# Performance work log

Hardware: AMD Instinct MI355X
Metric: run time of the kernel (lower is better)

Reference implementation:

```python
import jax, jax.numpy as jnp
import numpy as np

AGENT_RADIUS = 0.2
SAFETY_DIST = 0.1
_ang = np.linspace(0.0, 2.0 * np.pi, 8, endpoint=False)
OBSTACLES = np.stack([10.0 * np.cos(_ang), 10.0 * np.sin(_ang), 0.5 * np.ones(8)], axis=-1).astype(np.float32)  # (x, y, r)


def _qp_solve(p, G, h):
    """Exact solve of: min_z 0.5 z^T z + p^T z  s.t. G z <= h, z in R^2.
    Equivalent to QPFunction with Q=I. Enumerates KKT candidates over active
    sets of size 0, 1, 2 (closed form in 2D) and picks the feasible optimum.
    p: [2], G: [m,2], h: [m]."""
    m = G.shape[0]
    ii, jj = np.triu_indices(m, 1)
    # active set {} -> unconstrained minimizer
    z0 = -p[None, :]                                        # [1,2]
    # active set {i}: z = -p - lam*g_i, g_i.z = h_i
    gg = jnp.sum(G * G, axis=-1)                            # [m]
    lam1 = (-(G @ p) - h) / (gg + 1e-12)
    z1 = -p[None, :] - lam1[:, None] * G                    # [m,2]
    ok1 = lam1 >= -1e-8
    # active set {i,j}: z solves 2x2 system [g_i; g_j] z = [h_i; h_j]
    Gi, Gj = G[ii], G[jj]                                   # [P,2]
    hi, hj = h[ii], h[jj]
    det = Gi[:, 0] * Gj[:, 1] - Gi[:, 1] * Gj[:, 0]
    det_ok = jnp.abs(det) > 1e-9
    ds = jnp.where(det_ok, det, 1.0)
    zx = (hi * Gj[:, 1] - hj * Gi[:, 1]) / ds
    zy = (Gi[:, 0] * hj - Gj[:, 0] * hi) / ds
    z2 = jnp.stack([zx, zy], axis=-1)                       # [P,2]
    r = -(z2 + p[None, :])                                  # A^T lam = r
    lam_i = (Gj[:, 1] * r[:, 0] - Gj[:, 0] * r[:, 1]) / ds
    lam_j = (Gi[:, 0] * r[:, 1] - Gi[:, 1] * r[:, 0]) / ds
    ok2 = det_ok & (lam_i >= -1e-8) & (lam_j >= -1e-8)
    Z = jnp.concatenate([z0, z1, z2], axis=0)               # [K,2]
    ok = jnp.concatenate([jnp.ones((1,), bool), ok1, ok2], axis=0)
    tol = 1e-6 * (1.0 + jnp.abs(h))
    feas = jnp.all(Z @ G.T <= (h + tol)[None, :], axis=-1)  # [K]
    obj = 0.5 * jnp.sum(Z * Z, axis=-1) + Z @ p
    obj = jnp.where(ok & feas, obj, jnp.inf)
    return Z[jnp.argmin(obj)]


def _forward(x, mean, std, W1, b1, W21, b21, W31, b31, W22, b22, W32, b32):
    x0 = x * std + mean                                     # de-normalized state [B,8]
    hid = jax.nn.relu(x @ W1.T + b1)
    x31 = jax.nn.relu(hid @ W21.T + b21) @ W31.T + b31      # reference control p [B,2]
    x32 = 4.0 * jax.nn.sigmoid(jax.nn.relu(hid @ W22.T + b22) @ W32.T + b32)  # CBF penalties [B,2]
    px, py, theta, v = x0[:, 0], x0[:, 1], x0[:, 2], x0[:, 3]
    ox, oy, oth, ov = x0[:, 4], x0[:, 5], x0[:, 6], x0[:, 7]
    st, ct = jnp.sin(theta), jnp.cos(theta)
    vs, vc = v * st, v * ct
    obs = jnp.asarray(OBSTACLES, x.dtype)
    # static obstacle constraints, vectorized over the n_obs obstacles
    dx = px[:, None] - obs[None, :, 0]                      # [B,n_obs]
    dy = py[:, None] - obs[None, :, 1]
    R = AGENT_RADIUS + obs[:, 2] + SAFETY_DIST
    bar = dx * dx + dy * dy - (R * R)[None, :]
    bdot = 2.0 * dx * vc[:, None] + 2.0 * dy * vs[:, None]
    Lf2b = (2.0 * v * v)[:, None]
    u1 = -2.0 * dx * vs[:, None] + 2.0 * dy * vc[:, None]
    u2 = 2.0 * dx * ct[:, None] + 2.0 * dy * st[:, None]
    G_obs = -jnp.stack([u1, u2], axis=-1)                   # [B,n_obs,2]
    s0, s1 = x32[:, 0:1], x32[:, 1:2]
    h_obs = Lf2b + (s0 + s1) * bdot + (s0 * s1) * bar       # [B,n_obs]
    # opponent constraint
    Ro = 2.0 * AGENT_RADIUS + SAFETY_DIST
    dxo, dyo = px - ox, py - oy
    so, co = jnp.sin(oth), jnp.cos(oth)
    bar_o = dxo * dxo + dyo * dyo - Ro * Ro
    bdot_o = 2.0 * dxo * (vc - ov * co) + 2.0 * dyo * (vs - ov * so)
    Lf2b_o = 2.0 * (v * v + ov * ov + 2.0 * v * ov * jnp.cos(theta - oth))
    u1o = -2.0 * dxo * vs + 2.0 * dyo * vc
    u2o = 2.0 * dxo * ct + 2.0 * dyo * st
    G_opp = -jnp.stack([u1o, u2o], axis=-1)[:, None, :]     # [B,1,2]
    h_opp = (Lf2b_o + (x32[:, 0] + x32[:, 1]) * bdot_o + x32[:, 0] * x32[:, 1] * bar_o)[:, None]
    G = jnp.concatenate([G_obs, G_opp], axis=1)             # [B,m,2]
    h = jnp.concatenate([h_obs, h_opp], axis=1)             # [B,m]
    return jax.vmap(_qp_solve)(x31, G, h)                   # [B,2]


def setup_inputs() -> dict:
    key = jax.random.key(0)
    ks = jax.random.split(key, 6)
    B, nF, H1, H2 = 65536, 8, 256, 128

    def lin(k, o, i):
        k1, k2 = jax.random.split(k)
        W = jax.random.normal(k1, (o, i), jnp.float32) / np.float32(np.sqrt(i))
        b = jax.random.normal(k2, (o,), jnp.float32) * 0.01
        return W, b

    W1, b1 = lin(ks[0], H1, nF)
    W21, b21 = lin(ks[1], H2, H1)
    W31, b31 = lin(ks[2], 2, H2)
    W22, b22 = lin(ks[3], H2, H1)
    W32, b32 = lin(ks[4], 2, H2)
    x = jax.random.normal(ks[5], (B, nF), jnp.float32)
    return {"x": x, "mean": jnp.zeros((nF,), jnp.float32), "std": jnp.ones((nF,), jnp.float32),
            "W1": W1, "b1": b1, "W21": W21, "b21": b21, "W31": W31, "b31": b31,
            "W22": W22, "b22": b22, "W32": W32, "b32": b32, "sgn": 1}


def reference(x, mean, std, W1, b1, W21, b21, W31, b31, W22, b22, W32, b32, sgn):
    # sgn==1 / training path -> batched differentiable QP solve
    return _forward(x, mean, std, W1, b1, W21, b21, W31, b31, W22, b22, W32, b32)
```

## Files before the change

### kernel.cpp

```cpp
#include <hip/hip_runtime.h>
#include <math.h>


typedef unsigned int u32;
typedef unsigned short u16;
typedef __attribute__((ext_vector_type(8))) short short8;
typedef __attribute__((ext_vector_type(4))) float f32x4;
typedef __attribute__((ext_vector_type(2))) float f32x2;
typedef __attribute__((ext_vector_type(4))) u32 u32x4;

union Frag { short8 v; u32 u[4]; u32x4 q; };

__device__ __forceinline__ u16 f2bf(float f) {
    union { float f; u32 i; } v; v.f = f;
    u32 b = v.i;
    return (u16)((b + 0x7fffu + ((b >> 16) & 1u)) >> 16);
}
__device__ __forceinline__ u32 packbf(float a, float b) {
    return (u32)f2bf(a) | ((u32)f2bf(b) << 16);
}

__device__ const float OBX[8] = { 10.f, 7.07106781186547524f, 6.123234e-16f, -7.07106781186547524f,
                                 -10.f, -7.07106781186547524f, -1.8369702e-15f, 7.07106781186547524f };
__device__ const float OBY[8] = { 0.f, 7.07106781186547524f, 10.f, 7.07106781186547524f,
                                  1.2246468e-15f, -7.07106781186547524f, -10.f, -7.07106781186547524f };
__device__ const unsigned char PI_[36] = {0,0,0,0,0,0,0,0, 1,1,1,1,1,1,1, 2,2,2,2,2,2,
                                          3,3,3,3,3, 4,4,4,4, 5,5,5, 6,6, 7};
__device__ const unsigned char PJ_[36] = {1,2,3,4,5,6,7,8, 2,3,4,5,6,7,8, 3,4,5,6,7,8,
                                          4,5,6,7,8, 5,6,7,8, 6,7,8, 7,8, 8};

__global__ __launch_bounds__(256)
void prep_kernel(const float* __restrict__ W21, const float* __restrict__ W22,
                 u32* __restrict__ ws)
{
    int idx  = blockIdx.x * 256 + threadIdx.x;
    int lane = idx & 63;
    int nt   = (idx >> 6) & 7;
    int ks   = (idx >> 9) & 7;
    int head = idx >> 12;
    const float* W = head ? W22 : W21;
    int n  = nt * 16 + (lane & 15);
    int k0 = ks * 32 + (lane >> 4) * 8;
    const float* s = W + n * 256 + k0;
    u32x4 o;
    o.x = packbf(s[0], s[1]);
    o.y = packbf(s[2], s[3]);
    o.z = packbf(s[4], s[5]);
    o.w = packbf(s[6], s[7]);
    ((u32x4*)ws)[idx] = o;
}

__global__ __launch_bounds__(256)
void barriernet_kernel(const float* __restrict__ x,
                       const float* __restrict__ meanp,
                       const float* __restrict__ stdp,
                       const float* __restrict__ W1,
                       const float* __restrict__ b1,
                       const float* __restrict__ b21,
                       const float* __restrict__ W31,
                       const float* __restrict__ b31,
                       const float* __restrict__ b22,
                       const float* __restrict__ W32,
                       const float* __restrict__ b32,
                       const u32* __restrict__ wsB,
                       float* __restrict__ out, int Btot)
{
    const int tid  = threadIdx.x;
    const int wave = tid >> 6;
    const int lane = tid & 63;
    const int q    = lane >> 4;
    const int m    = lane & 15;
    const int blockRow = blockIdx.x * 128;
    const int waveRow  = blockRow + wave * 32;

    __shared__ f32x4 qC[9][128];
    __shared__ float lds_p[128][4];
    __shared__ f32x4 res[128];

    float xf0[8], xf1[8];
    {
        int R0 = waveRow + m, R1 = waveRow + 16 + m;
        const float* xp0 = x + (R0 < Btot ? R0 : 0) * 8;
        const float* xp1 = x + (R1 < Btot ? R1 : 0) * 8;
        #pragma unroll
        for (int c = 0; c < 8; ++c) { xf0[c] = xp0[c]; xf1[c] = xp1[c]; }
    }

    const f32x4* W1v = (const f32x4*)W1;
    const f32x4* b1v = (const f32x4*)b1;

    #pragma unroll 1
    for (int head = 0; head < 2; ++head) {
        const u32x4* Bb = (const u32x4*)wsB + head * 4096 + lane;
        const float* b2 = head ? b22 : b21;
        const float* W3 = head ? W32 : W31;
        const float* b3 = head ? b32 : b31;

        f32x4 acc[2][8];
        #pragma unroll
        for (int mt = 0; mt < 2; ++mt)
            #pragma unroll
            for (int nt = 0; nt < 8; ++nt) acc[mt][nt] = (f32x4){0.f, 0.f, 0.f, 0.f};

        #pragma unroll 1
        for (int ks = 0; ks < 8; ++ks) {
            int kb = ks * 32 + q * 8;
            f32x4 bA = b1v[kb >> 2];
            f32x4 bB = b1v[(kb >> 2) + 1];
            Frag A0, A1;
            float h0[8], h1[8];
            #pragma unroll
            for (int j = 0; j < 8; ++j) {
                f32x4 wa = W1v[(kb + j) * 2];
                f32x4 wb = W1v[(kb + j) * 2 + 1];
                float bj = (j < 4) ? bA[j] : bB[j - 4];
                float a0 = bj, a1 = bj;
                a0 = fmaf(wa.x, xf0[0], a0); a1 = fmaf(wa.x, xf1[0], a1);
                a0 = fmaf(wa.y, xf0[1], a0); a1 = fmaf(wa.y, xf1[1], a1);
                a0 = fmaf(wa.z, xf0[2], a0); a1 = fmaf(wa.z, xf1[2], a1);
                a0 = fmaf(wa.w, xf0[3], a0); a1 = fmaf(wa.w, xf1[3], a1);
                a0 = fmaf(wb.x, xf0[4], a0); a1 = fmaf(wb.x, xf1[4], a1);
                a0 = fmaf(wb.y, xf0[5], a0); a1 = fmaf(wb.y, xf1[5], a1);
                a0 = fmaf(wb.z, xf0[6], a0); a1 = fmaf(wb.z, xf1[6], a1);
                a0 = fmaf(wb.w, xf0[7], a0); a1 = fmaf(wb.w, xf1[7], a1);
                h0[j] = fmaxf(a0, 0.f);
                h1[j] = fmaxf(a1, 0.f);
            }
            #pragma unroll
            for (int t = 0; t < 4; ++t) {
                A0.u[t] = packbf(h0[2 * t], h0[2 * t + 1]);
                A1.u[t] = packbf(h1[2 * t], h1[2 * t + 1]);
            }
            const u32x4* Bks = Bb + ks * 512;
            #pragma unroll
            for (int nt = 0; nt < 8; ++nt) {
                Frag Bf; Bf.q = Bks[nt * 64];
                acc[0][nt] = __builtin_amdgcn_mfma_f32_16x16x32_bf16(A0.v, Bf.v, acc[0][nt], 0, 0, 0);
                acc[1][nt] = __builtin_amdgcn_mfma_f32_16x16x32_bf16(A1.v, Bf.v, acc[1][nt], 0, 0, 0);
            }
        }

        float pr0[2][4], pr1[2][4];
        #pragma unroll
        for (int mt = 0; mt < 2; ++mt)
            #pragma unroll
            for (int rg = 0; rg < 4; ++rg) { pr0[mt][rg] = 0.f; pr1[mt][rg] = 0.f; }
        #pragma unroll
        for (int nt = 0; nt < 8; ++nt) {
            int col = nt * 16 + m;
            float b2c = b2[col];
            float w0c = W3[col];
            float w1c = W3[128 + col];
            #pragma unroll
            for (int mt = 0; mt < 2; ++mt) {
                #pragma unroll
                for (int rg = 0; rg < 4; ++rg) {
                    float rv = fmaxf(acc[mt][nt][rg] + b2c, 0.f);
                    pr0[mt][rg] = fmaf(rv, w0c, pr0[mt][rg]);
                    pr1[mt][rg] = fmaf(rv, w1c, pr1[mt][rg]);
                }
            }
        }
        #pragma unroll
        for (int mt = 0; mt < 2; ++mt) {
            #pragma unroll
            for (int rg = 0; rg < 4; ++rg) {
                float v0 = pr0[mt][rg], v1 = pr1[mt][rg];
                #pragma unroll
                for (int off = 1; off < 16; off <<= 1) {
                    v0 += __shfl_xor(v0, off, 64);
                    v1 += __shfl_xor(v1, off, 64);
                }
                pr0[mt][rg] = v0; pr1[mt][rg] = v1;
            }
        }
        if (m == 0) {
            #pragma unroll
            for (int mt = 0; mt < 2; ++mt) {
                #pragma unroll
                for (int rg = 0; rg < 4; ++rg) {
                    int row = wave * 32 + mt * 16 + q * 4 + rg;
                    float a0 = pr0[mt][rg] + b3[0];
                    float a1 = pr1[mt][rg] + b3[1];
                    if (head == 0) {
                        lds_p[row][0] = a0;
                        lds_p[row][1] = a1;
                    } else {
                        lds_p[row][2] = 4.f / (1.f + expf(-a0));
                        lds_p[row][3] = 4.f / (1.f + expf(-a1));
                    }
                }
            }
        }
    }
    __syncthreads();

    const int rq   = tid & 127;
    const int half = tid >> 7;
    const int R    = blockRow + rq;
    float p0 = lds_p[rq][0];
    float p1 = lds_p[rq][1];

    if (half == 0) {
        float s0 = lds_p[rq][2];
        float s1 = lds_p[rq][3];
        float xr[8];
        const float* xp = x + (R < Btot ? R : 0) * 8;
        #pragma unroll
        for (int c = 0; c < 8; ++c) xr[c] = fmaf(xp[c], stdp[c], meanp[c]);
        float px = xr[0], py = xr[1], th = xr[2], v = xr[3];
        float ox = xr[4], oy = xr[5], oth = xr[6], ov = xr[7];
        float st = sinf(th),  ct = cosf(th);
        float so = sinf(oth), co = cosf(oth);
        float vs = v * st, vc = v * ct;
        float sps = s0 + s1, ss = s0 * s1;
        float Lf2b = 2.f * v * v;
        #pragma unroll 1
        for (int k = 0; k < 8; ++k) {
            float dx = px - OBX[k], dy = py - OBY[k];
            float bar  = dx * dx + dy * dy - 0.64f;
            float bdot = 2.f * dx * vc + 2.f * dy * vs;
            float gx = 2.f * dx * vs - 2.f * dy * vc;
            float gy = -(2.f * dx * ct + 2.f * dy * st);
            float hk = Lf2b + sps * bdot + ss * bar;
            float ht = hk + 1e-6f * (1.f + fabsf(hk));
            qC[k][rq] = (f32x4){gx, gy, hk, ht};
        }
        {
            float dxo = px - ox, dyo = py - oy;
            float bar_o  = dxo * dxo + dyo * dyo - 0.25f;
            float bdot_o = 2.f * dxo * (vc - ov * co) + 2.f * dyo * (vs - ov * so);
            float Lf2b_o = 2.f * (v * v + ov * ov + 2.f * v * ov * cosf(th - oth));
            float gx = 2.f * dxo * vs - 2.f * dyo * vc;
            float gy = -(2.f * dxo * ct + 2.f * dyo * st);
            float hk = Lf2b_o + sps * bdot_o + ss * bar_o;
            float ht = hk + 1e-6f * (1.f + fabsf(hk));
            qC[8][rq] = (f32x4){gx, gy, hk, ht};
        }
    }
    __syncthreads();

    const f32x4 C0 = qC[0][rq], C1 = qC[1][rq], C2 = qC[2][rq];
    const f32x4 C3 = qC[3][rq], C4 = qC[4][rq], C5 = qC[5][rq];
    const f32x4 C6 = qC[6][rq], C7 = qC[7][rq], C8 = qC[8][rq];

    const int c0i = half ? 23 : 0;
    const int c1i = half ? 46 : 23;
    float bobj = INFINITY;
    float bzx = -p0, bzy = -p1;
    #pragma unroll 2
    for (int c = c0i; c < c1i; ++c) {
        float zx, zy;
        bool pre;
        if (c == 0) {
            zx = -p0; zy = -p1; pre = true;
        } else if (c <= 9) {
            f32x4 g = qC[c - 1][rq];
            float gg  = g.x * g.x + g.y * g.y;
            float lam = (-(g.x * p0 + g.y * p1) - g.z) / (gg + 1e-12f);
            zx = -p0 - lam * g.x;
            zy = -p1 - lam * g.y;
            pre = (lam >= -1e-8f);
        } else {
            f32x4 gi = qC[PI_[c - 10]][rq];
            f32x4 gj = qC[PJ_[c - 10]][rq];
            float det = gi.x * gj.y - gi.y * gj.x;
            bool dok = fabsf(det) > 1e-9f;
            float ds = dok ? det : 1.0f;
            float inv = 1.0f / ds;
            zx = (gi.z * gj.y - gj.z * gi.y) * inv;
            zy = (gi.x * gj.z - gj.x * gi.z) * inv;
            float rx = -(zx + p0), ry = -(zy + p1);
            float li = (gj.y * rx - gj.x * ry) * inv;
            float lj = (gi.x * ry - gi.y * rx) * inv;
            pre = dok && (li >= -1e-8f) && (lj >= -1e-8f);
        }
        bool ok = pre;
        ok = ok && (zx * C0.x + zy * C0.y <= C0.w);
        ok = ok && (zx * C1.x + zy * C1.y <= C1.w);
        ok = ok && (zx * C2.x + zy * C2.y <= C2.w);
        ok = ok && (zx * C3.x + zy * C3.y <= C3.w);
        ok = ok && (zx * C4.x + zy * C4.y <= C4.w);
        ok = ok && (zx * C5.x + zy * C5.y <= C5.w);
        ok = ok && (zx * C6.x + zy * C6.y <= C6.w);
        ok = ok && (zx * C7.x + zy * C7.y <= C7.w);
        ok = ok && (zx * C8.x + zy * C8.y <= C8.w);
        float obj = 0.5f * (zx * zx + zy * zy) + zx * p0 + zy * p1;
        if (ok && obj < bobj) { bobj = obj; bzx = zx; bzy = zy; }
    }

    if (half) {
        res[rq] = (f32x4){bobj, bzx, bzy, 0.f};
    }
    __syncthreads();
    if (!half) {
        f32x4 r = res[rq];
        if (r.x < bobj) { bzx = r.y; bzy = r.z; }
        if (R < Btot) {
            f32x2 o2; o2.x = bzx; o2.y = bzy;
            ((f32x2*)out)[R] = o2;
        }
    }
}

extern "C" void kernel_launch(void* const* d_in, const int* in_sizes, int n_in,
                              void* d_out, int out_size, void* d_ws, size_t ws_size,
                              hipStream_t stream) {
    const float* x    = (const float*)d_in[0];
    const float* mean = (const float*)d_in[1];
    const float* stdv = (const float*)d_in[2];
    const float* W1   = (const float*)d_in[3];
    const float* b1   = (const float*)d_in[4];
    const float* W21  = (const float*)d_in[5];
    const float* b21  = (const float*)d_in[6];
    const float* W31  = (const float*)d_in[7];
    const float* b31  = (const float*)d_in[8];
    const float* W22  = (const float*)d_in[9];
    const float* b22  = (const float*)d_in[10];
    const float* W32  = (const float*)d_in[11];
    const float* b32  = (const float*)d_in[12];
    int B = in_sizes[0] / 8;
    float* out = (float*)d_out;
    u32* ws = (u32*)d_ws;

    hipLaunchKernelGGL(prep_kernel, dim3(32), dim3(256), 0, stream, W21, W22, ws);

    int blocks = (B + 127) / 128;
    hipLaunchKernelGGL(barriernet_kernel, dim3(blocks), dim3(256), 0, stream,
                       x, mean, stdv, W1, b1, b21, W31, b31, b22, W32, b32,
                       ws, out, B);
}
```

Baseline: 127.0 us.

## Split fused MLP+QP kernel into separate GEMM and QP kernels

```diff
diff --git a/kernel.cpp b/kernel.cpp
--- a/kernel.cpp
+++ b/kernel.cpp
@@ -3,6 +3,7 @@
 
 
 typedef unsigned int u32;
+typedef unsigned long long u64;
 typedef unsigned short u16;
 typedef __attribute__((ext_vector_type(8))) short short8;
 typedef __attribute__((ext_vector_type(4))) float f32x4;
@@ -24,10 +25,17 @@
                                  -10.f, -7.07106781186547524f, -1.8369702e-15f, 7.07106781186547524f };
 __device__ const float OBY[8] = { 0.f, 7.07106781186547524f, 10.f, 7.07106781186547524f,
                                   1.2246468e-15f, -7.07106781186547524f, -10.f, -7.07106781186547524f };
-__device__ const unsigned char PI_[36] = {0,0,0,0,0,0,0,0, 1,1,1,1,1,1,1, 2,2,2,2,2,2,
-                                          3,3,3,3,3, 4,4,4,4, 5,5,5, 6,6, 7};
-__device__ const unsigned char PJ_[36] = {1,2,3,4,5,6,7,8, 2,3,4,5,6,7,8, 3,4,5,6,7,8,
-                                          4,5,6,7,8, 5,6,7,8, 6,7,8, 7,8, 8};
+
+#define PI0_ 0x2111111100000000ULL
+#define PI1_ 0x5544443333322222ULL
+#define PI2_ 0x7665ULL
+#define PJ0_ 0x3876543287654321ULL
+#define PJ1_ 0x7687658765487654ULL
+#define PJ2_ 0x8878ULL
+__device__ __forceinline__ int unpack4(u64 w0, u64 w1, u64 w2, int t) {
+    u64 w = (t < 16) ? w0 : (t < 32) ? w1 : w2;
+    return (int)((w >> ((t & 15) * 4)) & 15);
+}
 
 __global__ __launch_bounds__(256)
 void prep_kernel(const float* __restrict__ W21, const float* __restrict__ W22,
@@ -51,19 +59,17 @@
 }
 
 __global__ __launch_bounds__(256)
-void barriernet_kernel(const float* __restrict__ x,
-                       const float* __restrict__ meanp,
-                       const float* __restrict__ stdp,
-                       const float* __restrict__ W1,
-                       const float* __restrict__ b1,
-                       const float* __restrict__ b21,
-                       const float* __restrict__ W31,
-                       const float* __restrict__ b31,
-                       const float* __restrict__ b22,
-                       const float* __restrict__ W32,
-                       const float* __restrict__ b32,
-                       const u32* __restrict__ wsB,
-                       float* __restrict__ out, int Btot)
+void gemm_kernel(const float* __restrict__ x,
+                 const float* __restrict__ W1,
+                 const float* __restrict__ b1,
+                 const float* __restrict__ b21,
+                 const float* __restrict__ W31,
+                 const float* __restrict__ b31,
+                 const float* __restrict__ b22,
+                 const float* __restrict__ W32,
+                 const float* __restrict__ b32,
+                 const u32* __restrict__ wsB,
+                 f32x4* __restrict__ ps, int Btot)
 {
     const int tid  = threadIdx.x;
     const int wave = tid >> 6;
@@ -73,9 +79,7 @@
     const int blockRow = blockIdx.x * 128;
     const int waveRow  = blockRow + wave * 32;
 
-    __shared__ f32x4 qC[9][128];
     __shared__ float lds_p[128][4];
-    __shared__ f32x4 res[128];
 
     float xf0[8], xf1[8];
     {
@@ -195,15 +199,33 @@
     }
     __syncthreads();
 
+    if (tid < 128) {
+        int R = blockRow + tid;
+        if (R < Btot) ps[R] = *(const f32x4*)lds_p[tid];
+    }
+}
+
+__global__ __launch_bounds__(256)
+void qp_kernel(const float* __restrict__ x,
+               const float* __restrict__ meanp,
+               const float* __restrict__ stdp,
+               const f32x4* __restrict__ ps,
+               float* __restrict__ out, int Btot)
+{
+    const int tid  = threadIdx.x;
     const int rq   = tid & 127;
     const int half = tid >> 7;
+    const int blockRow = blockIdx.x * 128;
     const int R    = blockRow + rq;
-    float p0 = lds_p[rq][0];
-    float p1 = lds_p[rq][1];
+
+    __shared__ f32x4 qC[9][128];
+    __shared__ f32x4 res[128];
+
+    f32x4 pv = ps[R < Btot ? R : 0];
+    float p0 = pv.x, p1 = pv.y;
 
     if (half == 0) {
-        float s0 = lds_p[rq][2];
-        float s1 = lds_p[rq][3];
+        float s0 = pv.z, s1 = pv.w;
         float xr[8];
         const float* xp = x + (R < Btot ? R : 0) * 8;
         #pragma unroll
@@ -262,8 +284,11 @@
             zy = -p1 - lam * g.y;
             pre = (lam >= -1e-8f);
         } else {
-            f32x4 gi = qC[PI_[c - 10]][rq];
-            f32x4 gj = qC[PJ_[c - 10]][rq];
+            int t = c - 10;
+            int pi = unpack4(PI0_, PI1_, PI2_, t);
+            int pj = unpack4(PJ0_, PJ1_, PJ2_, t);
+            f32x4 gi = qC[pi][rq];
+            f32x4 gj = qC[pj][rq];
             float det = gi.x * gj.y - gi.y * gj.x;
             bool dok = fabsf(det) > 1e-9f;
             float ds = dok ? det : 1.0f;
@@ -322,11 +347,13 @@
     int B = in_sizes[0] / 8;
     float* out = (float*)d_out;
     u32* ws = (u32*)d_ws;
+    f32x4* ps = (f32x4*)(ws + 32768);
 
     hipLaunchKernelGGL(prep_kernel, dim3(32), dim3(256), 0, stream, W21, W22, ws);
 
     int blocks = (B + 127) / 128;
-    hipLaunchKernelGGL(barriernet_kernel, dim3(blocks), dim3(256), 0, stream,
-                       x, mean, stdv, W1, b1, b21, W31, b31, b22, W32, b32,
-                       ws, out, B);
-}
+    hipLaunchKernelGGL(gemm_kernel, dim3(blocks), dim3(256), 0, stream,
+                       x, W1, b1, b21, W31, b31, b22, W32, b32, ws, ps, B);
+    hipLaunchKernelGGL(qp_kernel, dim3(blocks), dim3(256), 0, stream,
+                       x, mean, stdv, ps, out, B);
+}
```

Result: no change. 128.6 us (+1.2%).
